# Kernel tuning notes

Measured on AMD Instinct MI355X. Metric: run time of the kernel, lower is better.

## Reference

```python
import jax, jax.numpy as jnp
import numpy as np


def setup_inputs() -> dict:
    key = jax.random.key(0)
    k1, k2, k3 = jax.random.split(key, 3)
    B, L, C, H, W = 64, 64, 256, 8, 8
    z = jax.random.normal(k1, (B, L, C, H, W), dtype=jnp.float32)
    # KalmanFilter learned params: gain projection and state-transition (1x1 channel maps)
    W_gain = jax.random.normal(k2, (C, C), dtype=jnp.float32) * (1.0 / np.sqrt(C))
    b_gain = jnp.zeros((C,), dtype=jnp.float32)
    W_pred = jax.random.normal(k3, (C, C), dtype=jnp.float32) * (1.0 / np.sqrt(C))
    b_pred = jnp.zeros((C,), dtype=jnp.float32)
    return {"z": z, "W_gain": W_gain, "b_gain": b_gain, "W_pred": W_pred, "b_pred": b_pred}


def reference(z, W_gain, b_gain, W_pred, b_pred):
    # z: [B, L, C, H, W]
    # calc_gain: per-timestep 1x1 channel projection + sigmoid -> gain in (0,1)
    gain = jax.nn.sigmoid(
        jnp.einsum('oc,blchw->blohw', W_gain, z) + b_gain[:, None, None]
    )  # [B, L, C, H, W]

    def step(prev_z, inputs):
        z_i, k_i = inputs  # each [B, C, H, W]
        # predict on detached previous state (matches previous_z.detach())
        pz = jax.lax.stop_gradient(prev_z)
        z_prime = jnp.einsum('oc,bchw->bohw', W_pred, pz) + b_pred[:, None, None]
        # Kalman update: z_hat = z' + K * (z - z')
        z_hat = z_prime + k_i * (z_i - z_prime)
        return z_hat, None

    init = z[:, 0]  # step 0: z_hat = z[:, 0]
    z_seq = jnp.swapaxes(z[:, 1:], 0, 1)      # [L-1, B, C, H, W]
    k_seq = jnp.swapaxes(gain[:, 1:], 0, 1)   # [L-1, B, C, H, W]
    final, _ = jax.lax.scan(step, init, (z_seq, k_seq))
    return final  # [B, C, H, W]
```

## Files before the change

kernel.cpp:

```cpp
#include <hip/hip_runtime.h>

using f32x4  = __attribute__((ext_vector_type(4))) float;
using u16x8  = __attribute__((ext_vector_type(8))) unsigned short;
using u16x4  = __attribute__((ext_vector_type(4))) unsigned short;
using bf16x8 = __attribute__((ext_vector_type(8))) __bf16;

__device__ __forceinline__ unsigned short f2bf(float f){
  unsigned int u = __builtin_bit_cast(unsigned int, f);
  u += 0x7fffu + ((u >> 16) & 1u);
  return (unsigned short)(u >> 16);
}
__device__ __forceinline__ float bf2f(unsigned short h){
  return __builtin_bit_cast(float, ((unsigned int)h) << 16);
}
__device__ __forceinline__ unsigned short f2h(float f){
  return __builtin_bit_cast(unsigned short, (_Float16)f);
}
__device__ __forceinline__ float h2f(unsigned short h){
  return (float)__builtin_bit_cast(_Float16, h);
}
__device__ __forceinline__ f32x4 mfma_bf16(u16x8 a, u16x8 b, f32x4 c){
  return __builtin_amdgcn_mfma_f32_16x16x32_bf16(
      __builtin_bit_cast(bf16x8, a), __builtin_bit_cast(bf16x8, b), c, 0, 0, 0);
}
__device__ __forceinline__ float fast_sigmoid(float x){
  return __builtin_amdgcn_rcpf(1.0f + __builtin_amdgcn_exp2f(-1.44269504f * x));
}

constexpr int C_  = 256;
constexpr int L_  = 64;
constexpr int CHW = C_ * 64;


#define BAR_LDS() do {                                        \
    asm volatile("s_waitcnt lgkmcnt(0)" ::: "memory");        \
    __builtin_amdgcn_s_barrier();                             \
    asm volatile("" ::: "memory");                            \
  } while (0)

__global__ __launch_bounds__(512, 2)
void kalman_kernel(const float* __restrict__ z,  const float* __restrict__ Wg,
                   const float* __restrict__ bg, const float* __restrict__ Wp,
                   const float* __restrict__ bp, float* __restrict__ out)
{
  __shared__ unsigned short zbuf[4][4096];
  __shared__ unsigned short sbuf[2][4096];
  __shared__ unsigned short kbuf[2][4096];

  const int lx  = (int)blockIdx.x;
  const int xcd = lx & 7;
  const int loc = lx >> 3;
  const int b   = xcd + 8 * (loc >> 2);
  const int q   = loc & 3;

  const int t    = (int)threadIdx.x;
  const int lane = t & 63;
  const int wv   = t >> 6;
  const int role = wv >> 2;
  const int rw   = wv & 3;
  const int m    = lane & 15;
  const int g    = lane >> 4;

  const float* zg = z + (size_t)b * L_ * CHW + q * 16;

  const float* Wsel = (role == 0) ? Wp : Wg;
  const float* bsrc = (role == 0) ? bp : bg;
  u16x8 wf[4][8];
  f32x4 bsel[4];
  #pragma unroll
  for (int mi = 0; mi < 4; ++mi){
    const int mt = rw * 4 + mi;
    const float* src = Wsel + (size_t)(mt * 16 + m) * 256 + g * 8;
    #pragma unroll
    for (int kc = 0; kc < 8; ++kc){
      f32x4 a0 = *(const f32x4*)(src + kc * 32);
      f32x4 a1 = *(const f32x4*)(src + kc * 32 + 4);
      #pragma unroll
      for (int j = 0; j < 4; ++j){
        wf[mi][kc][j]     = f2bf(a0[j]);
        wf[mi][kc][j + 4] = f2bf(a1[j]);
      }
    }
    bsel[mi] = *(const f32x4*)(bsrc + (rw * 4 + mi) * 16 + g * 4);
  }

  const int sp = t & 15;
  const int ss = t >> 4;
  const float* st_src = zg + ss * 8 * 64 + sp;
  const int st_dst = (ss * 16 + sp) * 8;
  const int boff   = g * 128 + m * 8;

  {
    float v0[8], v1[8], v2[8];
    #pragma unroll
    for (int j = 0; j < 8; ++j) v0[j] = st_src[j * 64];
    #pragma unroll
    for (int j = 0; j < 8; ++j) v1[j] = st_src[CHW + j * 64];
    #pragma unroll
    for (int j = 0; j < 8; ++j) v2[j] = st_src[2 * CHW + j * 64];
    u16x8 u0, u1, u2;
    #pragma unroll
    for (int j = 0; j < 8; ++j){ u0[j] = f2bf(v0[j]); u1[j] = f2bf(v1[j]); u2[j] = f2bf(v2[j]); }
    *(u16x8*)(&sbuf[0][st_dst]) = u0;
    *(u16x8*)(&zbuf[1][st_dst]) = u1;
    *(u16x8*)(&zbuf[2][st_dst]) = u2;
  }
  float pf[8];
  const float* pfp = st_src + 3 * CHW;
  #pragma unroll
  for (int j = 0; j < 8; ++j) pf[j] = pfp[j * 64];
  pfp += CHW;
  __syncthreads();

  if (role == 1){
    u16x8 zf[8];
    #pragma unroll
    for (int kc = 0; kc < 8; ++kc) zf[kc] = *(const u16x8*)(&zbuf[1][kc * 512 + boff]);
    f32x4 gl[4] = {{0,0,0,0},{0,0,0,0},{0,0,0,0},{0,0,0,0}};
    #pragma unroll
    for (int kc = 0; kc < 8; ++kc)
      #pragma unroll
      for (int mi = 0; mi < 4; ++mi)
        gl[mi] = mfma_bf16(wf[mi][kc], zf[kc], gl[mi]);
    #pragma unroll
    for (int mi = 0; mi < 4; ++mi){
      const int ro = (rw * 4 + mi) * 16 + g * 4;
      const int el = ((ro >> 3) * 16 + m) * 8 + (ro & 7);
      u16x4 kk;
      #pragma unroll
      for (int r = 0; r < 4; ++r) kk[r] = f2h(fast_sigmoid(gl[mi][r] + bsel[mi][r]));
      *(u16x4*)(&kbuf[1][el]) = kk;
    }
  }
  __syncthreads();

  for (int l = 1; l < 63; ++l){
    if (l <= 61){
      u16x8 u;
      #pragma unroll
      for (int j = 0; j < 8; ++j) u[j] = f2bf(pf[j]);
      *(u16x8*)(&zbuf[(l + 2) & 3][st_dst]) = u;
    }
    if (l <= 60){
      #pragma unroll
      for (int j = 0; j < 8; ++j) pf[j] = pfp[j * 64];
      pfp += CHW;
    }

    if (role == 0){
      const unsigned short* sb  = sbuf[(l - 1) & 1];
      const unsigned short* zbl = zbuf[l & 3];
      const unsigned short* kb  = kbuf[l & 1];
      unsigned short* sbw = sbuf[l & 1];

      u16x4 zi4[4], k4[4];
      #pragma unroll
      for (int mi = 0; mi < 4; ++mi){
        const int ro = (rw * 4 + mi) * 16 + g * 4;
        const int el = ((ro >> 3) * 16 + m) * 8 + (ro & 7);
        zi4[mi] = *(const u16x4*)(zbl + el);
        k4[mi]  = *(const u16x4*)(kb + el);
      }
      u16x8 sf[8];
      #pragma unroll
      for (int kc = 0; kc < 8; ++kc) sf[kc] = *(const u16x8*)(sb + kc * 512 + boff);

      f32x4 zpA[4] = {{0,0,0,0},{0,0,0,0},{0,0,0,0},{0,0,0,0}};
      f32x4 zpB[4] = {{0,0,0,0},{0,0,0,0},{0,0,0,0},{0,0,0,0}};
      __builtin_amdgcn_s_setprio(1);
      #pragma unroll
      for (int kc = 0; kc < 4; ++kc)
        #pragma unroll
        for (int mi = 0; mi < 4; ++mi){
          zpA[mi] = mfma_bf16(wf[mi][kc],     sf[kc],     zpA[mi]);
          zpB[mi] = mfma_bf16(wf[mi][kc + 4], sf[kc + 4], zpB[mi]);
        }
      __builtin_amdgcn_s_setprio(0);

      #pragma unroll
      for (int mi = 0; mi < 4; ++mi){
        const int ro = (rw * 4 + mi) * 16 + g * 4;
        const int el = ((ro >> 3) * 16 + m) * 8 + (ro & 7);
        u16x4 sh;
        #pragma unroll
        for (int r = 0; r < 4; ++r){
          float zpr = zpA[mi][r] + zpB[mi][r] + bsel[mi][r];
          float zi  = bf2f(zi4[mi][r]);
          float zh  = zpr + h2f(k4[mi][r]) * (zi - zpr);
          sh[r] = f2bf(zh);
        }
        *(u16x4*)(sbw + el) = sh;
      }
    } else {
      const unsigned short* zb = zbuf[(l + 1) & 3];
      unsigned short* kw = kbuf[(l + 1) & 1];

      u16x8 zf[8];
      #pragma unroll
      for (int kc = 0; kc < 8; ++kc) zf[kc] = *(const u16x8*)(zb + kc * 512 + boff);

      f32x4 gl[4] = {{0,0,0,0},{0,0,0,0},{0,0,0,0},{0,0,0,0}};
      #pragma unroll
      for (int kc = 0; kc < 8; ++kc)
        #pragma unroll
        for (int mi = 0; mi < 4; ++mi)
          gl[mi] = mfma_bf16(wf[mi][kc], zf[kc], gl[mi]);

      #pragma unroll
      for (int mi = 0; mi < 4; ++mi){
        const int ro = (rw * 4 + mi) * 16 + g * 4;
        const int el = ((ro >> 3) * 16 + m) * 8 + (ro & 7);
        u16x4 kk;
        #pragma unroll
        for (int r = 0; r < 4; ++r) kk[r] = f2h(fast_sigmoid(gl[mi][r] + bsel[mi][r]));
        *(u16x4*)(kw + el) = kk;
      }
    }

    BAR_LDS();
  }

  if (role == 0){
    const unsigned short* sb  = sbuf[0];
    const unsigned short* zbl = zbuf[3];
    const unsigned short* kb  = kbuf[1];

    u16x4 zi4[4], k4[4];
    #pragma unroll
    for (int mi = 0; mi < 4; ++mi){
      const int ro = (rw * 4 + mi) * 16 + g * 4;
      const int el = ((ro >> 3) * 16 + m) * 8 + (ro & 7);
      zi4[mi] = *(const u16x4*)(zbl + el);
      k4[mi]  = *(const u16x4*)(kb + el);
    }
    u16x8 sf[8];
    #pragma unroll
    for (int kc = 0; kc < 8; ++kc) sf[kc] = *(const u16x8*)(sb + kc * 512 + boff);

    f32x4 zpA[4] = {{0,0,0,0},{0,0,0,0},{0,0,0,0},{0,0,0,0}};
    f32x4 zpB[4] = {{0,0,0,0},{0,0,0,0},{0,0,0,0},{0,0,0,0}};
    #pragma unroll
    for (int kc = 0; kc < 4; ++kc)
      #pragma unroll
      for (int mi = 0; mi < 4; ++mi){
        zpA[mi] = mfma_bf16(wf[mi][kc],     sf[kc],     zpA[mi]);
        zpB[mi] = mfma_bf16(wf[mi][kc + 4], sf[kc + 4], zpB[mi]);
      }

    #pragma unroll
    for (int mi = 0; mi < 4; ++mi){
      const int ro = (rw * 4 + mi) * 16 + g * 4;
      float* o = out + ((size_t)b * 256 + ro) * 64 + q * 16 + m;
      #pragma unroll
      for (int r = 0; r < 4; ++r){
        float zpr = zpA[mi][r] + zpB[mi][r] + bsel[mi][r];
        float zi  = bf2f(zi4[mi][r]);
        o[r * 64] = zpr + h2f(k4[mi][r]) * (zi - zpr);
      }
    }
  }
}

extern "C" void kernel_launch(void* const* d_in, const int* in_sizes, int n_in,
                              void* d_out, int out_size, void* d_ws, size_t ws_size,
                              hipStream_t stream)
{
  const float* z  = (const float*)d_in[0];
  const float* Wg = (const float*)d_in[1];
  const float* bg = (const float*)d_in[2];
  const float* Wp = (const float*)d_in[3];
  const float* bp = (const float*)d_in[4];
  float* out = (float*)d_out;
  hipLaunchKernelGGL(kalman_kernel, dim3(256), dim3(512), 0, stream,
                     z, Wg, bg, Wp, bp, out);
}
```

Baseline: 99.44 us.

## Replace per-step block barriers with LDS flag polling between producer and scan waves

Removes the block-wide barrier at every scan step. Gain-computing waves now run ahead as decoupled producers, publishing per-wave flags in LDS, while the scan waves poll only the flags they depend on. The gain waves handle two timesteps per iteration, take over all z staging (converting to bf16 in LDS), and kbuf grows to four slots so they can run further ahead. Bias is folded into the MFMA accumulator init. The change relies on volatile spin-polling with a bounded timeout, and on LDS write ordering through lgkmcnt waits rather than barriers, which risks subtle races.

```diff
diff --git a/kernel.cpp b/kernel.cpp
--- a/kernel.cpp
+++ b/kernel.cpp
@@ -31,12 +31,24 @@
 constexpr int L_  = 64;
 constexpr int CHW = C_ * 64;
 
-
-#define BAR_LDS() do {                                        \
-    asm volatile("s_waitcnt lgkmcnt(0)" ::: "memory");        \
-    __builtin_amdgcn_s_barrier();                             \
-    asm volatile("" ::: "memory");                            \
-  } while (0)
+#define LGKM0()    asm volatile("s_waitcnt lgkmcnt(0)" ::: "memory")
+#define MEMFENCE() asm volatile("" ::: "memory")
+
+__device__ __forceinline__ void poll4(const volatile int* f, int tgt){
+  int n = 0;
+  while (f[0] < tgt || f[1] < tgt || f[2] < tgt || f[3] < tgt){
+    if (++n > (1 << 24)) break;
+  }
+  MEMFENCE();
+}
+__device__ __forceinline__ void poll1(const volatile int* f, int tgt){
+  int n = 0;
+  while (f[0] < tgt){
+    if (++n > (1 << 24)) break;
+  }
+  MEMFENCE();
+}
+
 
 __global__ __launch_bounds__(512, 2)
 void kalman_kernel(const float* __restrict__ z,  const float* __restrict__ Wg,
@@ -45,13 +57,12 @@
 {
   __shared__ unsigned short zbuf[4][4096];
   __shared__ unsigned short sbuf[2][4096];
-  __shared__ unsigned short kbuf[2][4096];
+  __shared__ unsigned short kbuf[4][4096];
+  __shared__ int flg[16];
 
   const int lx  = (int)blockIdx.x;
-  const int xcd = lx & 7;
-  const int loc = lx >> 3;
-  const int b   = xcd + 8 * (loc >> 2);
-  const int q   = loc & 3;
+  const int b   = (lx & 7) + 8 * ((lx >> 3) >> 2);
+  const int q   = (lx >> 3) & 3;
 
   const int t    = (int)threadIdx.x;
   const int lane = t & 63;
@@ -81,91 +92,127 @@
         wf[mi][kc][j + 4] = f2bf(a1[j]);
       }
     }
-    bsel[mi] = *(const f32x4*)(bsrc + (rw * 4 + mi) * 16 + g * 4);
-  }
-
-  const int sp = t & 15;
-  const int ss = t >> 4;
-  const float* st_src = zg + ss * 8 * 64 + sp;
-  const int st_dst = (ss * 16 + sp) * 8;
-  const int boff   = g * 128 + m * 8;
+    bsel[mi] = *(const f32x4*)(bsrc + mt * 16 + g * 4);
+  }
 
   {
-    float v0[8], v1[8], v2[8];
-    #pragma unroll
-    for (int j = 0; j < 8; ++j) v0[j] = st_src[j * 64];
-    #pragma unroll
-    for (int j = 0; j < 8; ++j) v1[j] = st_src[CHW + j * 64];
-    #pragma unroll
-    for (int j = 0; j < 8; ++j) v2[j] = st_src[2 * CHW + j * 64];
-    u16x8 u0, u1, u2;
-    #pragma unroll
-    for (int j = 0; j < 8; ++j){ u0[j] = f2bf(v0[j]); u1[j] = f2bf(v1[j]); u2[j] = f2bf(v2[j]); }
-    *(u16x8*)(&sbuf[0][st_dst]) = u0;
-    *(u16x8*)(&zbuf[1][st_dst]) = u1;
-    *(u16x8*)(&zbuf[2][st_dst]) = u2;
-  }
-  float pf[8];
-  const float* pfp = st_src + 3 * CHW;
-  #pragma unroll
-  for (int j = 0; j < 8; ++j) pf[j] = pfp[j * 64];
-  pfp += CHW;
+    const int sp = t & 15;
+    const int ss = t >> 4;
+    const float* s0 = zg + ss * 8 * 64 + sp;
+    float v[8];
+    #pragma unroll
+    for (int j = 0; j < 8; ++j) v[j] = s0[j * 64];
+    u16x8 u;
+    #pragma unroll
+    for (int j = 0; j < 8; ++j) u[j] = f2bf(v[j]);
+    *(u16x8*)(&sbuf[0][(ss * 16 + sp) * 8]) = u;
+  }
+
+  const int sp2 = lane & 15;
+  const int so2 = rw * 4 + (lane >> 4);
+  const float* zsrc0 = zg + so2 * 8 * 64 + sp2;
+  const float* zsrc1 = zg + (so2 + 16) * 8 * 64 + sp2;
+  float pfA0[8], pfA1[8], pfB0[8], pfB1[8];
+  if (role == 1){
+    #pragma unroll
+    for (int i = 0; i < 8; ++i){
+      pfA0[i] = zsrc0[CHW + i * 64];     pfA1[i] = zsrc1[CHW + i * 64];
+      pfB0[i] = zsrc0[2 * CHW + i * 64]; pfB1[i] = zsrc1[2 * CHW + i * 64];
+    }
+  }
+
+  if (t < 16) flg[t] = 0;
   __syncthreads();
 
+  const int boff = g * 128 + m * 8;
+  volatile int* sflag  = (volatile int*)flg;
+  volatile int* gsflag = (volatile int*)(flg + 4);
+  volatile int* kflag  = (volatile int*)(flg + 8);
+
   if (role == 1){
-    u16x8 zf[8];
-    #pragma unroll
-    for (int kc = 0; kc < 8; ++kc) zf[kc] = *(const u16x8*)(&zbuf[1][kc * 512 + boff]);
-    f32x4 gl[4] = {{0,0,0,0},{0,0,0,0},{0,0,0,0},{0,0,0,0}};
-    #pragma unroll
-    for (int kc = 0; kc < 8; ++kc)
-      #pragma unroll
-      for (int mi = 0; mi < 4; ++mi)
-        gl[mi] = mfma_bf16(wf[mi][kc], zf[kc], gl[mi]);
-    #pragma unroll
-    for (int mi = 0; mi < 4; ++mi){
-      const int ro = (rw * 4 + mi) * 16 + g * 4;
-      const int el = ((ro >> 3) * 16 + m) * 8 + (ro & 7);
-      u16x4 kk;
-      #pragma unroll
-      for (int r = 0; r < 4; ++r) kk[r] = f2h(fast_sigmoid(gl[mi][r] + bsel[mi][r]));
-      *(u16x4*)(&kbuf[1][el]) = kk;
-    }
-  }
-  __syncthreads();
-
-  for (int l = 1; l < 63; ++l){
-    if (l <= 61){
-      u16x8 u;
-      #pragma unroll
-      for (int j = 0; j < 8; ++j) u[j] = f2bf(pf[j]);
-      *(u16x8*)(&zbuf[(l + 2) & 3][st_dst]) = u;
-    }
-    if (l <= 60){
-      #pragma unroll
-      for (int j = 0; j < 8; ++j) pf[j] = pfp[j * 64];
-      pfp += CHW;
-    }
-
-    if (role == 0){
-      const unsigned short* sb  = sbuf[(l - 1) & 1];
-      const unsigned short* zbl = zbuf[l & 3];
-      const unsigned short* kb  = kbuf[l & 1];
-      unsigned short* sbw = sbuf[l & 1];
+    for (int j = 1; j < 64; j += 2){
+      poll4(sflag, j - 3);
+
+      {
+        u16x8 u0, u1;
+        #pragma unroll
+        for (int i = 0; i < 8; ++i){ u0[i] = f2bf(pfA0[i]); u1[i] = f2bf(pfA1[i]); }
+        *(u16x8*)(&zbuf[j & 3][(so2 * 16 + sp2) * 8]) = u0;
+        *(u16x8*)(&zbuf[j & 3][((so2 + 16) * 16 + sp2) * 8]) = u1;
+      }
+      if (j + 1 < 64){
+        u16x8 u0, u1;
+        #pragma unroll
+        for (int i = 0; i < 8; ++i){ u0[i] = f2bf(pfB0[i]); u1[i] = f2bf(pfB1[i]); }
+        *(u16x8*)(&zbuf[(j + 1) & 3][(so2 * 16 + sp2) * 8]) = u0;
+        *(u16x8*)(&zbuf[(j + 1) & 3][((so2 + 16) * 16 + sp2) * 8]) = u1;
+      }
+      LGKM0();
+      if (lane == 0) gsflag[rw] = j;
+      poll4(gsflag, j);
+
+      if (j + 2 < 64){
+        const float* s0 = zsrc0 + (size_t)(j + 2) * CHW;
+        const float* s1 = zsrc1 + (size_t)(j + 2) * CHW;
+        #pragma unroll
+        for (int i = 0; i < 8; ++i){ pfA0[i] = s0[i * 64]; pfA1[i] = s1[i * 64]; }
+      }
+      if (j + 3 < 64){
+        const float* s0 = zsrc0 + (size_t)(j + 3) * CHW;
+        const float* s1 = zsrc1 + (size_t)(j + 3) * CHW;
+        #pragma unroll
+        for (int i = 0; i < 8; ++i){ pfB0[i] = s0[i * 64]; pfB1[i] = s1[i * 64]; }
+      }
+
+      #pragma unroll
+      for (int jj = 0; jj < 2; ++jj){
+        const int jc = j + jj;
+        if (jc > 63) break;
+        const unsigned short* zb = zbuf[jc & 3];
+        u16x8 zf[8];
+        #pragma unroll
+        for (int kc = 0; kc < 8; ++kc) zf[kc] = *(const u16x8*)(zb + kc * 512 + boff);
+        f32x4 gl[4] = {bsel[0], bsel[1], bsel[2], bsel[3]};
+        #pragma unroll
+        for (int kc = 0; kc < 8; ++kc)
+          #pragma unroll
+          for (int mi = 0; mi < 4; ++mi)
+            gl[mi] = mfma_bf16(wf[mi][kc], zf[kc], gl[mi]);
+        #pragma unroll
+        for (int mi = 0; mi < 4; ++mi){
+          const int ro = (rw * 4 + mi) * 16 + g * 4;
+          const int el = ((ro >> 3) * 16 + m) * 8 + (ro & 7);
+          u16x4 kk;
+          #pragma unroll
+          for (int r = 0; r < 4; ++r) kk[r] = f2h(fast_sigmoid(gl[mi][r]));
+          *(u16x4*)(&kbuf[jc & 3][el]) = kk;
+        }
+        LGKM0();
+        if (lane == 0) kflag[rw] = jc;
+      }
+    }
+  } else {
+    for (int l = 1; l < 63; ++l){
+      poll4(sflag, l - 1);
+      poll1(kflag + rw, l);
+
+      const unsigned short* sb = sbuf[(l - 1) & 1];
+      const unsigned short* zb = zbuf[l & 3];
+      const unsigned short* kb = kbuf[l & 3];
 
       u16x4 zi4[4], k4[4];
       #pragma unroll
       for (int mi = 0; mi < 4; ++mi){
         const int ro = (rw * 4 + mi) * 16 + g * 4;
         const int el = ((ro >> 3) * 16 + m) * 8 + (ro & 7);
-        zi4[mi] = *(const u16x4*)(zbl + el);
+        zi4[mi] = *(const u16x4*)(zb + el);
         k4[mi]  = *(const u16x4*)(kb + el);
       }
       u16x8 sf[8];
       #pragma unroll
       for (int kc = 0; kc < 8; ++kc) sf[kc] = *(const u16x8*)(sb + kc * 512 + boff);
 
-      f32x4 zpA[4] = {{0,0,0,0},{0,0,0,0},{0,0,0,0},{0,0,0,0}};
+      f32x4 zpA[4] = {bsel[0], bsel[1], bsel[2], bsel[3]};
       f32x4 zpB[4] = {{0,0,0,0},{0,0,0,0},{0,0,0,0},{0,0,0,0}};
       __builtin_amdgcn_s_setprio(1);
       #pragma unroll
@@ -177,6 +224,7 @@
         }
       __builtin_amdgcn_s_setprio(0);
 
+      unsigned short* sbw = sbuf[l & 1];
       #pragma unroll
       for (int mi = 0; mi < 4; ++mi){
         const int ro = (rw * 4 + mi) * 16 + g * 4;
@@ -184,60 +232,36 @@
         u16x4 sh;
         #pragma unroll
         for (int r = 0; r < 4; ++r){
-          float zpr = zpA[mi][r] + zpB[mi][r] + bsel[mi][r];
-          float zi  = bf2f(zi4[mi][r]);
-          float zh  = zpr + h2f(k4[mi][r]) * (zi - zpr);
+          float zpr = zpA[mi][r] + zpB[mi][r];
+          float zh  = zpr + h2f(k4[mi][r]) * (bf2f(zi4[mi][r]) - zpr);
           sh[r] = f2bf(zh);
         }
         *(u16x4*)(sbw + el) = sh;
       }
-    } else {
-      const unsigned short* zb = zbuf[(l + 1) & 3];
-      unsigned short* kw = kbuf[(l + 1) & 1];
-
-      u16x8 zf[8];
-      #pragma unroll
-      for (int kc = 0; kc < 8; ++kc) zf[kc] = *(const u16x8*)(zb + kc * 512 + boff);
-
-      f32x4 gl[4] = {{0,0,0,0},{0,0,0,0},{0,0,0,0},{0,0,0,0}};
-      #pragma unroll
-      for (int kc = 0; kc < 8; ++kc)
-        #pragma unroll
-        for (int mi = 0; mi < 4; ++mi)
-          gl[mi] = mfma_bf16(wf[mi][kc], zf[kc], gl[mi]);
-
-      #pragma unroll
-      for (int mi = 0; mi < 4; ++mi){
-        const int ro = (rw * 4 + mi) * 16 + g * 4;
-        const int el = ((ro >> 3) * 16 + m) * 8 + (ro & 7);
-        u16x4 kk;
-        #pragma unroll
-        for (int r = 0; r < 4; ++r) kk[r] = f2h(fast_sigmoid(gl[mi][r] + bsel[mi][r]));
-        *(u16x4*)(kw + el) = kk;
-      }
-    }
-
-    BAR_LDS();
-  }
-
-  if (role == 0){
-    const unsigned short* sb  = sbuf[0];
-    const unsigned short* zbl = zbuf[3];
-    const unsigned short* kb  = kbuf[1];
+      LGKM0();
+      if (lane == 0) sflag[rw] = l;
+    }
+
+    poll4(sflag, 62);
+    poll1(kflag + rw, 63);
+
+    const unsigned short* sb = sbuf[0];
+    const unsigned short* zb = zbuf[3];
+    const unsigned short* kb = kbuf[3];
 
     u16x4 zi4[4], k4[4];
     #pragma unroll
     for (int mi = 0; mi < 4; ++mi){
       const int ro = (rw * 4 + mi) * 16 + g * 4;
       const int el = ((ro >> 3) * 16 + m) * 8 + (ro & 7);
-      zi4[mi] = *(const u16x4*)(zbl + el);
+      zi4[mi] = *(const u16x4*)(zb + el);
       k4[mi]  = *(const u16x4*)(kb + el);
     }
     u16x8 sf[8];
     #pragma unroll
     for (int kc = 0; kc < 8; ++kc) sf[kc] = *(const u16x8*)(sb + kc * 512 + boff);
 
-    f32x4 zpA[4] = {{0,0,0,0},{0,0,0,0},{0,0,0,0},{0,0,0,0}};
+    f32x4 zpA[4] = {bsel[0], bsel[1], bsel[2], bsel[3]};
     f32x4 zpB[4] = {{0,0,0,0},{0,0,0,0},{0,0,0,0},{0,0,0,0}};
     #pragma unroll
     for (int kc = 0; kc < 4; ++kc)
@@ -253,9 +277,8 @@
       float* o = out + ((size_t)b * 256 + ro) * 64 + q * 16 + m;
       #pragma unroll
       for (int r = 0; r < 4; ++r){
-        float zpr = zpA[mi][r] + zpB[mi][r] + bsel[mi][r];
-        float zi  = bf2f(zi4[mi][r]);
-        o[r * 64] = zpr + h2f(k4[mi][r]) * (zi - zpr);
+        float zpr = zpA[mi][r] + zpB[mi][r];
+        o[r * 64] = zpr + h2f(k4[mi][r]) * (bf2f(zi4[mi][r]) - zpr);
       }
     }
   }
```

New measurement: 139.9 us. +40.7%, slower.

## Move z prefetch staging to gain waves and fold bias into MFMA accumulators

Applied to the files above, without the earlier changes.

The global prefetch and bf16 staging of future z timesteps move from all waves to only the gain-role waves, each of which now handles two slices, so the recurrent prediction waves on the critical path do no global loads. Bias is preloaded into the MFMA accumulators instead of being added afterward. The f32-to-bf16 conversion now uses the native __bf16 cast, and the state-fragment LDS reads are issued earlier. This shortens the serial recurrence at the cost of more registers and global latency on the gain waves.

```diff
diff --git a/kernel.cpp b/kernel.cpp
--- a/kernel.cpp
+++ b/kernel.cpp
@@ -6,9 +6,7 @@
 using bf16x8 = __attribute__((ext_vector_type(8))) __bf16;
 
 __device__ __forceinline__ unsigned short f2bf(float f){
-  unsigned int u = __builtin_bit_cast(unsigned int, f);
-  u += 0x7fffu + ((u >> 16) & 1u);
-  return (unsigned short)(u >> 16);
+  return __builtin_bit_cast(unsigned short, (__bf16)f);
 }
 __device__ __forceinline__ float bf2f(unsigned short h){
   return __builtin_bit_cast(float, ((unsigned int)h) << 16);
@@ -30,13 +28,13 @@
 constexpr int C_  = 256;
 constexpr int L_  = 64;
 constexpr int CHW = C_ * 64;
-
 
 #define BAR_LDS() do {                                        \
     asm volatile("s_waitcnt lgkmcnt(0)" ::: "memory");        \
     __builtin_amdgcn_s_barrier();                             \
     asm volatile("" ::: "memory");                            \
   } while (0)
+
 
 __global__ __launch_bounds__(512, 2)
 void kalman_kernel(const float* __restrict__ z,  const float* __restrict__ Wg,
@@ -48,10 +46,8 @@
   __shared__ unsigned short kbuf[2][4096];
 
   const int lx  = (int)blockIdx.x;
-  const int xcd = lx & 7;
-  const int loc = lx >> 3;
-  const int b   = xcd + 8 * (loc >> 2);
-  const int q   = loc & 3;
+  const int b   = (lx & 7) + 8 * ((lx >> 3) >> 2);
+  const int q   = (lx >> 3) & 3;
 
   const int t    = (int)threadIdx.x;
   const int lane = t & 63;
@@ -73,50 +69,52 @@
     const float* src = Wsel + (size_t)(mt * 16 + m) * 256 + g * 8;
     #pragma unroll
     for (int kc = 0; kc < 8; ++kc){
-      f32x4 a0 = *(const f32x4*)(src + kc * 32);
-      f32x4 a1 = *(const f32x4*)(src + kc * 32 + 4);
-      #pragma unroll
-      for (int j = 0; j < 4; ++j){
-        wf[mi][kc][j]     = f2bf(a0[j]);
-        wf[mi][kc][j + 4] = f2bf(a1[j]);
-      }
-    }
-    bsel[mi] = *(const f32x4*)(bsrc + (rw * 4 + mi) * 16 + g * 4);
-  }
-
-  const int sp = t & 15;
-  const int ss = t >> 4;
-  const float* st_src = zg + ss * 8 * 64 + sp;
-  const int st_dst = (ss * 16 + sp) * 8;
-  const int boff   = g * 128 + m * 8;
+      #pragma unroll
+      for (int j = 0; j < 8; ++j) wf[mi][kc][j] = f2bf(src[kc * 32 + j]);
+    }
+    bsel[mi] = *(const f32x4*)(bsrc + mt * 16 + g * 4);
+  }
 
   {
-    float v0[8], v1[8], v2[8];
-    #pragma unroll
-    for (int j = 0; j < 8; ++j) v0[j] = st_src[j * 64];
-    #pragma unroll
-    for (int j = 0; j < 8; ++j) v1[j] = st_src[CHW + j * 64];
-    #pragma unroll
-    for (int j = 0; j < 8; ++j) v2[j] = st_src[2 * CHW + j * 64];
+    const int sp = t & 15;
+    const int ss = t >> 4;
+    const float* s0 = zg + ss * 8 * 64 + sp;
+    const int dst = (ss * 16 + sp) * 8;
     u16x8 u0, u1, u2;
     #pragma unroll
-    for (int j = 0; j < 8; ++j){ u0[j] = f2bf(v0[j]); u1[j] = f2bf(v1[j]); u2[j] = f2bf(v2[j]); }
-    *(u16x8*)(&sbuf[0][st_dst]) = u0;
-    *(u16x8*)(&zbuf[1][st_dst]) = u1;
-    *(u16x8*)(&zbuf[2][st_dst]) = u2;
-  }
-  float pf[8];
-  const float* pfp = st_src + 3 * CHW;
-  #pragma unroll
-  for (int j = 0; j < 8; ++j) pf[j] = pfp[j * 64];
-  pfp += CHW;
+    for (int j = 0; j < 8; ++j){
+      u0[j] = f2bf(s0[j * 64]);
+      u1[j] = f2bf(s0[CHW + j * 64]);
+      u2[j] = f2bf(s0[2 * CHW + j * 64]);
+    }
+    *(u16x8*)(&sbuf[0][dst]) = u0;
+    *(u16x8*)(&zbuf[1][dst]) = u1;
+    *(u16x8*)(&zbuf[2][dst]) = u2;
+  }
+
+  const int sp2 = lane & 15;
+  const int so2 = rw * 4 + (lane >> 4);
+  const float* zsrc0 = zg + so2 * 8 * 64 + sp2;
+  const float* zsrc1 = zg + (so2 + 16) * 8 * 64 + sp2;
+  const float* pf0 = zsrc0 + 4 * (size_t)CHW;
+  const float* pf1 = zsrc1 + 4 * (size_t)CHW;
+  float pfA[8], pfB[8];
+  if (role == 1){
+    #pragma unroll
+    for (int i = 0; i < 8; ++i){
+      pfA[i] = zsrc0[3 * CHW + i * 64];
+      pfB[i] = zsrc1[3 * CHW + i * 64];
+    }
+  }
   __syncthreads();
+
+  const int boff = g * 128 + m * 8;
 
   if (role == 1){
     u16x8 zf[8];
     #pragma unroll
     for (int kc = 0; kc < 8; ++kc) zf[kc] = *(const u16x8*)(&zbuf[1][kc * 512 + boff]);
-    f32x4 gl[4] = {{0,0,0,0},{0,0,0,0},{0,0,0,0},{0,0,0,0}};
+    f32x4 gl[4] = {bsel[0], bsel[1], bsel[2], bsel[3]};
     #pragma unroll
     for (int kc = 0; kc < 8; ++kc)
       #pragma unroll
@@ -128,31 +126,22 @@
       const int el = ((ro >> 3) * 16 + m) * 8 + (ro & 7);
       u16x4 kk;
       #pragma unroll
-      for (int r = 0; r < 4; ++r) kk[r] = f2h(fast_sigmoid(gl[mi][r] + bsel[mi][r]));
+      for (int r = 0; r < 4; ++r) kk[r] = f2h(fast_sigmoid(gl[mi][r]));
       *(u16x4*)(&kbuf[1][el]) = kk;
     }
   }
   __syncthreads();
 
   for (int l = 1; l < 63; ++l){
-    if (l <= 61){
-      u16x8 u;
-      #pragma unroll
-      for (int j = 0; j < 8; ++j) u[j] = f2bf(pf[j]);
-      *(u16x8*)(&zbuf[(l + 2) & 3][st_dst]) = u;
-    }
-    if (l <= 60){
-      #pragma unroll
-      for (int j = 0; j < 8; ++j) pf[j] = pfp[j * 64];
-      pfp += CHW;
-    }
-
     if (role == 0){
       const unsigned short* sb  = sbuf[(l - 1) & 1];
       const unsigned short* zbl = zbuf[l & 3];
       const unsigned short* kb  = kbuf[l & 1];
       unsigned short* sbw = sbuf[l & 1];
 
+      u16x8 sf[8];
+      #pragma unroll
+      for (int kc = 0; kc < 8; ++kc) sf[kc] = *(const u16x8*)(sb + kc * 512 + boff);
       u16x4 zi4[4], k4[4];
       #pragma unroll
       for (int mi = 0; mi < 4; ++mi){
@@ -161,11 +150,8 @@
         zi4[mi] = *(const u16x4*)(zbl + el);
         k4[mi]  = *(const u16x4*)(kb + el);
       }
-      u16x8 sf[8];
-      #pragma unroll
-      for (int kc = 0; kc < 8; ++kc) sf[kc] = *(const u16x8*)(sb + kc * 512 + boff);
-
-      f32x4 zpA[4] = {{0,0,0,0},{0,0,0,0},{0,0,0,0},{0,0,0,0}};
+
+      f32x4 zpA[4] = {bsel[0], bsel[1], bsel[2], bsel[3]};
       f32x4 zpB[4] = {{0,0,0,0},{0,0,0,0},{0,0,0,0},{0,0,0,0}};
       __builtin_amdgcn_s_setprio(1);
       #pragma unroll
@@ -184,9 +170,8 @@
         u16x4 sh;
         #pragma unroll
         for (int r = 0; r < 4; ++r){
-          float zpr = zpA[mi][r] + zpB[mi][r] + bsel[mi][r];
-          float zi  = bf2f(zi4[mi][r]);
-          float zh  = zpr + h2f(k4[mi][r]) * (zi - zpr);
+          float zpr = zpA[mi][r] + zpB[mi][r];
+          float zh  = zpr + h2f(k4[mi][r]) * (bf2f(zi4[mi][r]) - zpr);
           sh[r] = f2bf(zh);
         }
         *(u16x4*)(sbw + el) = sh;
@@ -199,7 +184,14 @@
       #pragma unroll
       for (int kc = 0; kc < 8; ++kc) zf[kc] = *(const u16x8*)(zb + kc * 512 + boff);
 
-      f32x4 gl[4] = {{0,0,0,0},{0,0,0,0},{0,0,0,0},{0,0,0,0}};
+      float nA[8], nB[8];
+      if (l <= 60){
+        #pragma unroll
+        for (int i = 0; i < 8; ++i){ nA[i] = pf0[i * 64]; nB[i] = pf1[i * 64]; }
+        pf0 += CHW; pf1 += CHW;
+      }
+
+      f32x4 gl[4] = {bsel[0], bsel[1], bsel[2], bsel[3]};
       #pragma unroll
       for (int kc = 0; kc < 8; ++kc)
         #pragma unroll
@@ -212,8 +204,20 @@
         const int el = ((ro >> 3) * 16 + m) * 8 + (ro & 7);
         u16x4 kk;
         #pragma unroll
-        for (int r = 0; r < 4; ++r) kk[r] = f2h(fast_sigmoid(gl[mi][r] + bsel[mi][r]));
+        for (int r = 0; r < 4; ++r) kk[r] = f2h(fast_sigmoid(gl[mi][r]));
         *(u16x4*)(kw + el) = kk;
+      }
+
+      if (l <= 61){
+        u16x8 u0, u1;
+        #pragma unroll
+        for (int i = 0; i < 8; ++i){ u0[i] = f2bf(pfA[i]); u1[i] = f2bf(pfB[i]); }
+        *(u16x8*)(&zbuf[(l + 2) & 3][(so2 * 16 + sp2) * 8]) = u0;
+        *(u16x8*)(&zbuf[(l + 2) & 3][((so2 + 16) * 16 + sp2) * 8]) = u1;
+      }
+      if (l <= 60){
+        #pragma unroll
+        for (int i = 0; i < 8; ++i){ pfA[i] = nA[i]; pfB[i] = nB[i]; }
       }
     }
 
@@ -225,6 +229,9 @@
     const unsigned short* zbl = zbuf[3];
     const unsigned short* kb  = kbuf[1];
 
+    u16x8 sf[8];
+    #pragma unroll
+    for (int kc = 0; kc < 8; ++kc) sf[kc] = *(const u16x8*)(sb + kc * 512 + boff);
     u16x4 zi4[4], k4[4];
     #pragma unroll
     for (int mi = 0; mi < 4; ++mi){
@@ -233,11 +240,8 @@
       zi4[mi] = *(const u16x4*)(zbl + el);
       k4[mi]  = *(const u16x4*)(kb + el);
     }
-    u16x8 sf[8];
-    #pragma unroll
-    for (int kc = 0; kc < 8; ++kc) sf[kc] = *(const u16x8*)(sb + kc * 512 + boff);
-
-    f32x4 zpA[4] = {{0,0,0,0},{0,0,0,0},{0,0,0,0},{0,0,0,0}};
+
+    f32x4 zpA[4] = {bsel[0], bsel[1], bsel[2], bsel[3]};
     f32x4 zpB[4] = {{0,0,0,0},{0,0,0,0},{0,0,0,0},{0,0,0,0}};
     #pragma unroll
     for (int kc = 0; kc < 4; ++kc)
@@ -253,9 +257,8 @@
       float* o = out + ((size_t)b * 256 + ro) * 64 + q * 16 + m;
       #pragma unroll
       for (int r = 0; r < 4; ++r){
-        float zpr = zpA[mi][r] + zpB[mi][r] + bsel[mi][r];
-        float zi  = bf2f(zi4[mi][r]);
-        o[r * 64] = zpr + h2f(k4[mi][r]) * (zi - zpr);
+        float zpr = zpA[mi][r] + zpB[mi][r];
+        o[r * 64] = zpr + h2f(k4[mi][r]) * (bf2f(zi4[mi][r]) - zpr);
       }
     }
   }
```

Result: slower. 137.7 us (+38.5%).
